# Optimization experiments

Measured on AMD Instinct MI355X. Metric: run time of the kernel, lower is better.

## Reference

```python
import jax, jax.numpy as jnp
import numpy as np

N_NODES = 50000
N_EDGES = 800000
DIM = 128
N_LAYERS = 5


def setup_inputs() -> dict:
    key = jax.random.key(0)
    k1, k2, k3, k4 = jax.random.split(key, 4)
    x = jax.random.normal(k1, (N_NODES, DIM), dtype=jnp.float32)
    edge_index = jax.random.randint(k2, (2, N_EDGES), 0, N_NODES, dtype=jnp.int64)
    # He-ish scale for stacked GCN layers so activations stay sane
    weights = jax.random.normal(k3, (N_LAYERS, DIM, DIM), dtype=jnp.float32) / jnp.sqrt(jnp.float32(DIM))
    biases = jax.random.normal(k4, (N_LAYERS, DIM), dtype=jnp.float32) * 0.01
    return {"x": x, "edge_index": edge_index, "weights": weights, "biases": biases}


def reference(x, edge_index, weights, biases):
    """5x (GCNConv -> ReLU). GCNConv: out = D^-1/2 (A+I) D^-1/2 (x W) + b."""
    n = x.shape[0]
    src, dst = edge_index[0], edge_index[1]
    # add self-loops (PyG GCNConv default)
    loop = jnp.arange(n, dtype=src.dtype)
    src_f = jnp.concatenate([src, loop])
    dst_f = jnp.concatenate([dst, loop])
    # symmetric normalization based on in-degree (incl. self loops)
    deg = jax.ops.segment_sum(jnp.ones(src_f.shape[0], dtype=x.dtype), dst_f, num_segments=n)
    dinv = jnp.where(deg > 0, jax.lax.rsqrt(deg), 0.0)
    norm = dinv[src_f] * dinv[dst_f]  # [E+N]

    for l in range(weights.shape[0]):
        h = x @ weights[l]                      # [N, D] dense transform
        msg = h[src_f] * norm[:, None]          # gather + scale  [E+N, D]
        x = jax.ops.segment_sum(msg, dst_f, num_segments=n) + biases[l]
        x = jax.nn.relu(x)
    return x
```

## Files before the change

kernel.cpp:

```cpp
#include <hip/hip_runtime.h>
#include <hip/hip_bf16.h>
#include <hip/hip_fp16.h>


#define GCN_DIM 128

typedef short bf16x8 __attribute__((ext_vector_type(8)));
typedef float f32x4 __attribute__((ext_vector_type(4)));

__device__ __forceinline__ unsigned short f2bf(float f) {
    unsigned int u = __float_as_uint(f);
    u += 0x7FFFu + ((u >> 16) & 1u);
    return (unsigned short)(u >> 16);
}
__device__ __forceinline__ float bf2f(unsigned short b) {
    return __uint_as_float(((unsigned int)b) << 16);
}
__device__ __forceinline__ float bflo(unsigned int p) { return __uint_as_float(p << 16); }
__device__ __forceinline__ float bfhi(unsigned int p) { return __uint_as_float(p & 0xFFFF0000u); }

__global__ void count_kernel(const int* __restrict__ dst, int* __restrict__ cnt,
                             int* __restrict__ rank, int E) {
    int e = blockIdx.x * 256 + threadIdx.x;
    if (e < E) rank[e] = atomicAdd(&cnt[dst[e]], 1);
}

__global__ __launch_bounds__(256) void scan_part_kernel(const int* __restrict__ cnt,
                                                        int* __restrict__ loc,
                                                        int* __restrict__ bsum, int n) {
    __shared__ int s[256];
    int t = threadIdx.x;
    int i0 = blockIdx.x * 1024 + t * 4;
    int v0 = (i0 + 0 < n) ? cnt[i0 + 0] : 0;
    int v1 = (i0 + 1 < n) ? cnt[i0 + 1] : 0;
    int v2 = (i0 + 2 < n) ? cnt[i0 + 2] : 0;
    int v3 = (i0 + 3 < n) ? cnt[i0 + 3] : 0;
    int tsum = v0 + v1 + v2 + v3;
    s[t] = tsum;
    __syncthreads();
    for (int d = 1; d < 256; d <<= 1) {
        int u = (t >= d) ? s[t - d] : 0;
        __syncthreads();
        s[t] += u;
        __syncthreads();
    }
    int base = s[t] - tsum;
    if (i0 + 0 < n) loc[i0 + 0] = base; base += v0;
    if (i0 + 1 < n) loc[i0 + 1] = base; base += v1;
    if (i0 + 2 < n) loc[i0 + 2] = base; base += v2;
    if (i0 + 3 < n) loc[i0 + 3] = base;
    if (t == 255) bsum[blockIdx.x] = s[255];
}

__global__ __launch_bounds__(256) void scan_top_kernel(int* __restrict__ bsum, int nb) {
    __shared__ int s[256];
    int t = threadIdx.x;
    int v = (t < nb) ? bsum[t] : 0;
    s[t] = v;
    __syncthreads();
    for (int d = 1; d < 256; d <<= 1) {
        int u = (t >= d) ? s[t - d] : 0;
        __syncthreads();
        s[t] += u;
        __syncthreads();
    }
    if (t < nb) bsum[t] = s[t] - v;
}

__global__ void scan_add_kernel(int* __restrict__ offs,
                                const int* __restrict__ bsum, const int* __restrict__ cnt,
                                float* __restrict__ dinv, int n, int E) {
    int i = blockIdx.x * 256 + threadIdx.x;
    if (i < n) {
        offs[i] = offs[i] + bsum[i >> 10];
        dinv[i] = rsqrtf((float)cnt[i] + 1.0f);
    }
    if (i == 0) offs[n] = E;
}

__global__ void fill_kernel(const int* __restrict__ src, const int* __restrict__ dst,
                            const float* __restrict__ dinv, const int* __restrict__ rank,
                            const int* __restrict__ offs,
                            unsigned int* __restrict__ edat, int E) {
    int e = blockIdx.x * 256 + threadIdx.x;
    if (e < E) {
        int d = dst[e];
        int s = src[e];
        int p = offs[d] + rank[e];
        unsigned short wb = __half_as_ushort(__float2half(dinv[s]));
        edat[p] = (unsigned int)s | ((unsigned int)wb << 16);
    }
}

__global__ void split_x_kernel(const float* __restrict__ x, unsigned short* __restrict__ xh,
                               unsigned short* __restrict__ xl, int total) {
    int i = (blockIdx.x * 256 + threadIdx.x) * 4;
    if (i >= total) return;
    float4 v = *(const float4*)&x[i];
    ushort4 h4, l4;
    h4.x = f2bf(v.x); l4.x = f2bf(v.x - bf2f(h4.x));
    h4.y = f2bf(v.y); l4.y = f2bf(v.y - bf2f(h4.y));
    h4.z = f2bf(v.z); l4.z = f2bf(v.z - bf2f(h4.z));
    h4.w = f2bf(v.w); l4.w = f2bf(v.w - bf2f(h4.w));
    *(ushort4*)&xh[i] = h4;
    *(ushort4*)&xl[i] = l4;
}

__global__ void wsplit_kernel(const float* __restrict__ Wall, unsigned short* __restrict__ Wfh,
                              unsigned short* __restrict__ Wfl, int total) {
    int idx = blockIdx.x * 256 + threadIdx.x;
    if (idx >= total) return;
    int l = idx >> 14;
    int rem = idx & 16383;
    int k = rem >> 7;
    int nn = rem & 127;
    float v = Wall[idx];
    unsigned short hi = f2bf(v);
    unsigned short lo = f2bf(v - bf2f(hi));
    int t = nn >> 4, ln = nn & 15;
    int ks = k >> 5, q = (k >> 3) & 3, j = k & 7;
    int o = ((((l << 5) | (t << 2) | ks) << 6) | (q << 4) | ln) * 8 + j;
    Wfh[o] = hi;
    Wfl[o] = lo;
}

__global__ __launch_bounds__(256) void gemm_mfma_kernel(
    const unsigned short* __restrict__ xh, const unsigned short* __restrict__ xl,
    const unsigned short* __restrict__ Wfh, const unsigned short* __restrict__ Wfl,
    unsigned short* __restrict__ h, int n) {
    __shared__ unsigned short ldsW[2][8192];
    int tid = threadIdx.x;
    int wave = tid >> 6, lane = tid & 63;
    int q = lane >> 4, ln = lane & 15;
    int rowbase = blockIdx.x * 64 + wave * 16;
    bf16x8 A[4][2];
    {
        int ar = rowbase + ln;
        if (ar >= n) ar = n - 1;
        size_t base = (size_t)ar * GCN_DIM;
#pragma unroll
        for (int ks = 0; ks < 4; ks++) {
            A[ks][0] = *(const bf16x8*)&xh[base + ks * 32 + q * 8];
            A[ks][1] = *(const bf16x8*)&xl[base + ks * 32 + q * 8];
        }
    }
    int node = rowbase + ln;
#pragma unroll
    for (int half = 0; half < 2; half++) {
        if (half) __syncthreads();
        {
            const uint4* gh = (const uint4*)(Wfh + half * 8192);
            const uint4* gl = (const uint4*)(Wfl + half * 8192);
            uint4* sh = (uint4*)ldsW[0];
            uint4* sl = (uint4*)ldsW[1];
#pragma unroll
            for (int r = 0; r < 4; r++) {
                sh[tid + 256 * r] = gh[tid + 256 * r];
                sl[tid + 256 * r] = gl[tid + 256 * r];
            }
        }
        __syncthreads();
#pragma unroll
        for (int tp = 0; tp < 2; tp++) {
            int tta = tp * 2, ttb = tp * 2 + 1;
            f32x4 accA = (f32x4)(0.f), accB = (f32x4)(0.f);
#pragma unroll
            for (int ks = 0; ks < 4; ks++) {
                int foA = ((tta * 4 + ks) * 64 + lane) * 8;
                int foB = ((ttb * 4 + ks) * 64 + lane) * 8;
                bf16x8 bhA = *(const bf16x8*)&ldsW[0][foA];
                bf16x8 blA = *(const bf16x8*)&ldsW[1][foA];
                bf16x8 bhB = *(const bf16x8*)&ldsW[0][foB];
                bf16x8 blB = *(const bf16x8*)&ldsW[1][foB];
                accA = __builtin_amdgcn_mfma_f32_16x16x32_bf16(bhA, A[ks][0], accA, 0, 0, 0);
                accB = __builtin_amdgcn_mfma_f32_16x16x32_bf16(bhB, A[ks][0], accB, 0, 0, 0);
                accA = __builtin_amdgcn_mfma_f32_16x16x32_bf16(bhA, A[ks][1], accA, 0, 0, 0);
                accB = __builtin_amdgcn_mfma_f32_16x16x32_bf16(bhB, A[ks][1], accB, 0, 0, 0);
                accA = __builtin_amdgcn_mfma_f32_16x16x32_bf16(blA, A[ks][0], accA, 0, 0, 0);
                accB = __builtin_amdgcn_mfma_f32_16x16x32_bf16(blB, A[ks][0], accB, 0, 0, 0);
            }
            if (node < n) {
                int ta = half * 4 + tta, tb = half * 4 + ttb;
                ushort4 oA, oB;
                oA.x = f2bf(accA[0]); oA.y = f2bf(accA[1]);
                oA.z = f2bf(accA[2]); oA.w = f2bf(accA[3]);
                oB.x = f2bf(accB[0]); oB.y = f2bf(accB[1]);
                oB.z = f2bf(accB[2]); oB.w = f2bf(accB[3]);
                *(ushort4*)&h[((size_t)ta * n + node) * 16 + q * 4] = oA;
                *(ushort4*)&h[((size_t)tb * n + node) * 16 + q * 4] = oB;
            }
        }
    }
}

__global__ __launch_bounds__(256) void agg_kernel(
    const unsigned short* __restrict__ h,
    const unsigned int* __restrict__ edat,
    const int* __restrict__ offs,
    const float* __restrict__ dinv, const float* __restrict__ bias,
    unsigned short* __restrict__ xh_out,
    unsigned short* __restrict__ xl_out,
    float* __restrict__ fout, int n) {
    int tid = threadIdx.x;
    int wave = tid >> 6, lane = tid & 63;
    int sub = lane >> 3, ln = lane & 7;
    int slice = blockIdx.x & 7;
    int node = (blockIdx.x >> 3) * 32 + wave * 8 + sub;
    if (node >= n) return;
    size_t sbase = (size_t)slice * n;
    int fo = ln * 2;
    float di = dinv[node];
    unsigned int sp = *(const unsigned int*)&h[(sbase + node) * 16 + fo];
    float ax0 = di * bflo(sp), ay0 = di * bfhi(sp);
    float ax1 = 0.f, ay1 = 0.f, ax2 = 0.f, ay2 = 0.f, ax3 = 0.f, ay3 = 0.f;
    int s = offs[node], e = offs[node + 1];
    int j = s;
    for (; j + 8 <= e; j += 8) {
        unsigned int v0 = edat[j], v1 = edat[j + 1], v2 = edat[j + 2], v3 = edat[j + 3];
        unsigned int v4 = edat[j + 4], v5 = edat[j + 5], v6 = edat[j + 6], v7 = edat[j + 7];
        unsigned int p0 = *(const unsigned int*)&h[(sbase + (v0 & 0xFFFFu)) * 16 + fo];
        unsigned int p1 = *(const unsigned int*)&h[(sbase + (v1 & 0xFFFFu)) * 16 + fo];
        unsigned int p2 = *(const unsigned int*)&h[(sbase + (v2 & 0xFFFFu)) * 16 + fo];
        unsigned int p3 = *(const unsigned int*)&h[(sbase + (v3 & 0xFFFFu)) * 16 + fo];
        unsigned int p4 = *(const unsigned int*)&h[(sbase + (v4 & 0xFFFFu)) * 16 + fo];
        unsigned int p5 = *(const unsigned int*)&h[(sbase + (v5 & 0xFFFFu)) * 16 + fo];
        unsigned int p6 = *(const unsigned int*)&h[(sbase + (v6 & 0xFFFFu)) * 16 + fo];
        unsigned int p7 = *(const unsigned int*)&h[(sbase + (v7 & 0xFFFFu)) * 16 + fo];
        float w0 = __half2float(__ushort_as_half((unsigned short)(v0 >> 16)));
        float w1 = __half2float(__ushort_as_half((unsigned short)(v1 >> 16)));
        float w2 = __half2float(__ushort_as_half((unsigned short)(v2 >> 16)));
        float w3 = __half2float(__ushort_as_half((unsigned short)(v3 >> 16)));
        float w4 = __half2float(__ushort_as_half((unsigned short)(v4 >> 16)));
        float w5 = __half2float(__ushort_as_half((unsigned short)(v5 >> 16)));
        float w6 = __half2float(__ushort_as_half((unsigned short)(v6 >> 16)));
        float w7 = __half2float(__ushort_as_half((unsigned short)(v7 >> 16)));
        ax0 = fmaf(w0, bflo(p0), ax0); ay0 = fmaf(w0, bfhi(p0), ay0);
        ax1 = fmaf(w1, bflo(p1), ax1); ay1 = fmaf(w1, bfhi(p1), ay1);
        ax2 = fmaf(w2, bflo(p2), ax2); ay2 = fmaf(w2, bfhi(p2), ay2);
        ax3 = fmaf(w3, bflo(p3), ax3); ay3 = fmaf(w3, bfhi(p3), ay3);
        ax0 = fmaf(w4, bflo(p4), ax0); ay0 = fmaf(w4, bfhi(p4), ay0);
        ax1 = fmaf(w5, bflo(p5), ax1); ay1 = fmaf(w5, bfhi(p5), ay1);
        ax2 = fmaf(w6, bflo(p6), ax2); ay2 = fmaf(w6, bfhi(p6), ay2);
        ax3 = fmaf(w7, bflo(p7), ax3); ay3 = fmaf(w7, bfhi(p7), ay3);
    }
    for (; j + 4 <= e; j += 4) {
        unsigned int v0 = edat[j], v1 = edat[j + 1], v2 = edat[j + 2], v3 = edat[j + 3];
        unsigned int p0 = *(const unsigned int*)&h[(sbase + (v0 & 0xFFFFu)) * 16 + fo];
        unsigned int p1 = *(const unsigned int*)&h[(sbase + (v1 & 0xFFFFu)) * 16 + fo];
        unsigned int p2 = *(const unsigned int*)&h[(sbase + (v2 & 0xFFFFu)) * 16 + fo];
        unsigned int p3 = *(const unsigned int*)&h[(sbase + (v3 & 0xFFFFu)) * 16 + fo];
        float w0 = __half2float(__ushort_as_half((unsigned short)(v0 >> 16)));
        float w1 = __half2float(__ushort_as_half((unsigned short)(v1 >> 16)));
        float w2 = __half2float(__ushort_as_half((unsigned short)(v2 >> 16)));
        float w3 = __half2float(__ushort_as_half((unsigned short)(v3 >> 16)));
        ax0 = fmaf(w0, bflo(p0), ax0); ay0 = fmaf(w0, bfhi(p0), ay0);
        ax1 = fmaf(w1, bflo(p1), ax1); ay1 = fmaf(w1, bfhi(p1), ay1);
        ax2 = fmaf(w2, bflo(p2), ax2); ay2 = fmaf(w2, bfhi(p2), ay2);
        ax3 = fmaf(w3, bflo(p3), ax3); ay3 = fmaf(w3, bfhi(p3), ay3);
    }
    for (; j < e; j++) {
        unsigned int v0 = edat[j];
        unsigned int p0 = *(const unsigned int*)&h[(sbase + (v0 & 0xFFFFu)) * 16 + fo];
        float w0 = __half2float(__ushort_as_half((unsigned short)(v0 >> 16)));
        ax0 = fmaf(w0, bflo(p0), ax0);
        ay0 = fmaf(w0, bfhi(p0), ay0);
    }
    float ax = (ax0 + ax1) + (ax2 + ax3);
    float ay = (ay0 + ay1) + (ay2 + ay3);
    int cg = slice * 16 + fo;
    float2 b = *(const float2*)&bias[cg];
    float rx = fmaxf(fmaf(di, ax, b.x), 0.f);
    float ry = fmaxf(fmaf(di, ay, b.y), 0.f);
    if (fout) {
        unsigned long long pv = (unsigned long long)__float_as_uint(rx) |
                                ((unsigned long long)__float_as_uint(ry) << 32);
        __builtin_nontemporal_store(pv, (unsigned long long*)&fout[(size_t)node * GCN_DIM + cg]);
    } else {
        unsigned short hx = f2bf(rx), hy = f2bf(ry);
        unsigned int hp = (unsigned int)hx | ((unsigned int)hy << 16);
        unsigned short lx = f2bf(rx - bf2f(hx)), ly = f2bf(ry - bf2f(hy));
        unsigned int lp = (unsigned int)lx | ((unsigned int)ly << 16);
        __builtin_nontemporal_store(hp, (unsigned int*)&xh_out[(size_t)node * GCN_DIM + cg]);
        __builtin_nontemporal_store(lp, (unsigned int*)&xl_out[(size_t)node * GCN_DIM + cg]);
    }
}

extern "C" void kernel_launch(void* const* d_in, const int* in_sizes, int n_in,
                              void* d_out, int out_size, void* d_ws, size_t ws_size,
                              hipStream_t stream) {
    const float* x0    = (const float*)d_in[0];
    const int*   edges = (const int*)d_in[1];
    const float* Wall  = (const float*)d_in[2];
    const float* Ball  = (const float*)d_in[3];
    float* out = (float*)d_out;

    const int n = in_sizes[0] / GCN_DIM;
    const int E = in_sizes[1] / 2;
    const int L = in_sizes[2] / (GCN_DIM * GCN_DIM);

    int*   cnt    = (int*)d_ws;
    float* dinv   = (float*)(cnt + n);
    int*   offs   = (int*)(dinv + n);
    int*   bsum   = offs + n + 16;
    int*   rank   = bsum + 64;
    unsigned int* edat = (unsigned int*)(rank + E);
    unsigned short* h   = (unsigned short*)(edat + E);
    unsigned short* xh  = h  + (size_t)n * GCN_DIM;
    unsigned short* xl  = xh + (size_t)n * GCN_DIM;
    unsigned short* Wfh = xl + (size_t)n * GCN_DIM;
    unsigned short* Wfl = Wfh + (size_t)L * GCN_DIM * GCN_DIM;

    const int* src = edges;
    const int* dst = edges + E;

    int nb_n = (n + 255) / 256;
    int nb_e = (E + 255) / 256;
    int nb_scan = (n + 1023) / 1024;

    hipMemsetAsync(cnt, 0, (size_t)n * sizeof(int), stream);
    count_kernel<<<nb_e, 256, 0, stream>>>(dst, cnt, rank, E);
    scan_part_kernel<<<nb_scan, 256, 0, stream>>>(cnt, offs, bsum, n);
    scan_top_kernel<<<1, 256, 0, stream>>>(bsum, nb_scan);
    scan_add_kernel<<<nb_n, 256, 0, stream>>>(offs, bsum, cnt, dinv, n, E);
    fill_kernel<<<nb_e, 256, 0, stream>>>(src, dst, dinv, rank, offs, edat, E);

    int xtotal = n * GCN_DIM;
    split_x_kernel<<<(xtotal / 4 + 255) / 256, 256, 0, stream>>>(x0, xh, xl, xtotal);
    int wtotal = L * GCN_DIM * GCN_DIM;
    wsplit_kernel<<<(wtotal + 255) / 256, 256, 0, stream>>>(Wall, Wfh, Wfl, wtotal);

    int gemm_blocks = (n + 63) / 64;
    int agg_blocks  = ((n + 31) / 32) * 8;

    for (int l = 0; l < L; l++) {
        gemm_mfma_kernel<<<gemm_blocks, 256, 0, stream>>>(
            xh, xl, Wfh + (size_t)l * GCN_DIM * GCN_DIM, Wfl + (size_t)l * GCN_DIM * GCN_DIM, h, n);
        agg_kernel<<<agg_blocks, 256, 0, stream>>>(
            h, edat, offs, dinv, Ball + (size_t)l * GCN_DIM,
            xh, xl, (l == L - 1) ? out : nullptr, n);
    }
}
```

Measured before the change: 414.2 us.

## Sort nodes by degree for aggregation and interleave hi/lo activation splits

Adds a counting sort of nodes by in-degree (capped at 127), so each aggregation wave handles nodes of similar degree and lanes within a wave diverge less. The bf16 hi/lo activation halves are interleaved into one buffer with 32-element chunks per slice, so the aggregation write and the GEMM A-load touch nearby memory. This costs three extra setup kernels and an indirection through the order array, and output stores become scattered by node id.

```diff
diff --git a/kernel.cpp b/kernel.cpp
--- a/kernel.cpp
+++ b/kernel.cpp
@@ -92,8 +92,52 @@
     }
 }
 
-__global__ void split_x_kernel(const float* __restrict__ x, unsigned short* __restrict__ xh,
-                               unsigned short* __restrict__ xl, int total) {
+__global__ __launch_bounds__(256) void dhist_kernel(const int* __restrict__ cnt,
+                                                    int* __restrict__ dhist,
+                                                    int* __restrict__ drank, int n) {
+    __shared__ int lhist[128];
+    __shared__ int lbase[128];
+    int t = threadIdx.x;
+    if (t < 128) lhist[t] = 0;
+    __syncthreads();
+    int i = blockIdx.x * 256 + t;
+    int d = 0, lr = 0;
+    if (i < n) {
+        d = min(cnt[i], 127);
+        lr = atomicAdd(&lhist[d], 1);
+    }
+    __syncthreads();
+    if (t < 128) lbase[t] = (lhist[t] > 0) ? atomicAdd(&dhist[t], lhist[t]) : 0;
+    __syncthreads();
+    if (i < n) drank[i] = lbase[d] + lr;
+}
+
+__global__ __launch_bounds__(128) void dscan_kernel(int* __restrict__ dhist) {
+    __shared__ int s[128];
+    int t = threadIdx.x;
+    int v = dhist[t];
+    s[t] = v;
+    __syncthreads();
+    for (int d = 1; d < 128; d <<= 1) {
+        int u = (t >= d) ? s[t - d] : 0;
+        __syncthreads();
+        s[t] += u;
+        __syncthreads();
+    }
+    dhist[t] = s[t] - v;
+}
+
+__global__ void dorder_kernel(const int* __restrict__ cnt, const int* __restrict__ dhist,
+                              const int* __restrict__ drank, int* __restrict__ order, int n) {
+    int i = blockIdx.x * 256 + threadIdx.x;
+    if (i < n) {
+        int d = min(cnt[i], 127);
+        order[dhist[d] + drank[i]] = i;
+    }
+}
+
+__global__ void split_x_kernel(const float* __restrict__ x, unsigned short* __restrict__ xs,
+                               int total) {
     int i = (blockIdx.x * 256 + threadIdx.x) * 4;
     if (i >= total) return;
     float4 v = *(const float4*)&x[i];
@@ -102,8 +146,11 @@
     h4.y = f2bf(v.y); l4.y = f2bf(v.y - bf2f(h4.y));
     h4.z = f2bf(v.z); l4.z = f2bf(v.z - bf2f(h4.z));
     h4.w = f2bf(v.w); l4.w = f2bf(v.w - bf2f(h4.w));
-    *(ushort4*)&xh[i] = h4;
-    *(ushort4*)&xl[i] = l4;
+    int node = i >> 7, k = i & 127;
+    int s = k >> 4, within = k & 15;
+    size_t base = (size_t)node * 256 + s * 32 + within;
+    *(ushort4*)&xs[base] = h4;
+    *(ushort4*)&xs[base + 16] = l4;
 }
 
 __global__ void wsplit_kernel(const float* __restrict__ Wall, unsigned short* __restrict__ Wfh,
@@ -125,7 +172,7 @@
 }
 
 __global__ __launch_bounds__(256) void gemm_mfma_kernel(
-    const unsigned short* __restrict__ xh, const unsigned short* __restrict__ xl,
+    const unsigned short* __restrict__ xs,
     const unsigned short* __restrict__ Wfh, const unsigned short* __restrict__ Wfl,
     unsigned short* __restrict__ h, int n) {
     __shared__ unsigned short ldsW[2][8192];
@@ -137,11 +184,13 @@
     {
         int ar = rowbase + ln;
         if (ar >= n) ar = n - 1;
-        size_t base = (size_t)ar * GCN_DIM;
+        size_t base = (size_t)ar * 256;
 #pragma unroll
         for (int ks = 0; ks < 4; ks++) {
-            A[ks][0] = *(const bf16x8*)&xh[base + ks * 32 + q * 8];
-            A[ks][1] = *(const bf16x8*)&xl[base + ks * 32 + q * 8];
+            int s = 2 * ks + (q >> 1);
+            int within = (q & 1) * 8;
+            A[ks][0] = *(const bf16x8*)&xs[base + s * 32 + within];
+            A[ks][1] = *(const bf16x8*)&xs[base + s * 32 + 16 + within];
         }
     }
     int node = rowbase + ln;
@@ -198,15 +247,16 @@
     const unsigned int* __restrict__ edat,
     const int* __restrict__ offs,
     const float* __restrict__ dinv, const float* __restrict__ bias,
-    unsigned short* __restrict__ xh_out,
-    unsigned short* __restrict__ xl_out,
+    const int* __restrict__ order,
+    unsigned short* __restrict__ xs_out,
     float* __restrict__ fout, int n) {
     int tid = threadIdx.x;
     int wave = tid >> 6, lane = tid & 63;
     int sub = lane >> 3, ln = lane & 7;
     int slice = blockIdx.x & 7;
-    int node = (blockIdx.x >> 3) * 32 + wave * 8 + sub;
-    if (node >= n) return;
+    int g = (blockIdx.x >> 3) * 32 + wave * 8 + sub;
+    if (g >= n) return;
+    int node = order[g];
     size_t sbase = (size_t)slice * n;
     int fo = ln * 2;
     float di = dinv[node];
@@ -280,8 +330,9 @@
         unsigned int hp = (unsigned int)hx | ((unsigned int)hy << 16);
         unsigned short lx = f2bf(rx - bf2f(hx)), ly = f2bf(ry - bf2f(hy));
         unsigned int lp = (unsigned int)lx | ((unsigned int)ly << 16);
-        __builtin_nontemporal_store(hp, (unsigned int*)&xh_out[(size_t)node * GCN_DIM + cg]);
-        __builtin_nontemporal_store(lp, (unsigned int*)&xl_out[(size_t)node * GCN_DIM + cg]);
+        size_t ob = (size_t)node * 256 + slice * 32 + fo;
+        __builtin_nontemporal_store(hp, (unsigned int*)&xs_out[ob]);
+        __builtin_nontemporal_store(lp, (unsigned int*)&xs_out[ob + 16]);
     }
 }
 
@@ -299,15 +350,17 @@
     const int L = in_sizes[2] / (GCN_DIM * GCN_DIM);
 
     int*   cnt    = (int*)d_ws;
-    float* dinv   = (float*)(cnt + n);
+    int*   dhist  = cnt + n;
+    float* dinv   = (float*)(dhist + 128);
     int*   offs   = (int*)(dinv + n);
     int*   bsum   = offs + n + 16;
-    int*   rank   = bsum + 64;
+    int*   drank  = bsum + 64;
+    int*   order  = drank + n;
+    int*   rank   = order + n;
     unsigned int* edat = (unsigned int*)(rank + E);
     unsigned short* h   = (unsigned short*)(edat + E);
-    unsigned short* xh  = h  + (size_t)n * GCN_DIM;
-    unsigned short* xl  = xh + (size_t)n * GCN_DIM;
-    unsigned short* Wfh = xl + (size_t)n * GCN_DIM;
+    unsigned short* xs  = h  + (size_t)n * GCN_DIM;
+    unsigned short* Wfh = xs + (size_t)n * 256;
     unsigned short* Wfl = Wfh + (size_t)L * GCN_DIM * GCN_DIM;
 
     const int* src = edges;
@@ -317,15 +370,18 @@
     int nb_e = (E + 255) / 256;
     int nb_scan = (n + 1023) / 1024;
 
-    hipMemsetAsync(cnt, 0, (size_t)n * sizeof(int), stream);
+    hipMemsetAsync(cnt, 0, ((size_t)n + 128) * sizeof(int), stream);
     count_kernel<<<nb_e, 256, 0, stream>>>(dst, cnt, rank, E);
     scan_part_kernel<<<nb_scan, 256, 0, stream>>>(cnt, offs, bsum, n);
     scan_top_kernel<<<1, 256, 0, stream>>>(bsum, nb_scan);
     scan_add_kernel<<<nb_n, 256, 0, stream>>>(offs, bsum, cnt, dinv, n, E);
     fill_kernel<<<nb_e, 256, 0, stream>>>(src, dst, dinv, rank, offs, edat, E);
+    dhist_kernel<<<nb_n, 256, 0, stream>>>(cnt, dhist, drank, n);
+    dscan_kernel<<<1, 128, 0, stream>>>(dhist);
+    dorder_kernel<<<nb_n, 256, 0, stream>>>(cnt, dhist, drank, order, n);
 
     int xtotal = n * GCN_DIM;
-    split_x_kernel<<<(xtotal / 4 + 255) / 256, 256, 0, stream>>>(x0, xh, xl, xtotal);
+    split_x_kernel<<<(xtotal / 4 + 255) / 256, 256, 0, stream>>>(x0, xs, xtotal);
     int wtotal = L * GCN_DIM * GCN_DIM;
     wsplit_kernel<<<(wtotal + 255) / 256, 256, 0, stream>>>(Wall, Wfh, Wfl, wtotal);
 
@@ -334,9 +390,9 @@
 
     for (int l = 0; l < L; l++) {
         gemm_mfma_kernel<<<gemm_blocks, 256, 0, stream>>>(
-            xh, xl, Wfh + (size_t)l * GCN_DIM * GCN_DIM, Wfl + (size_t)l * GCN_DIM * GCN_DIM, h, n);
+            xs, Wfh + (size_t)l * GCN_DIM * GCN_DIM, Wfl + (size_t)l * GCN_DIM * GCN_DIM, h, n);
         agg_kernel<<<agg_blocks, 256, 0, stream>>>(
-            h, edat, offs, dinv, Ball + (size_t)l * GCN_DIM,
-            xh, xl, (l == L - 1) ? out : nullptr, n);
-    }
-}
+            h, edat, offs, dinv, Ball + (size_t)l * GCN_DIM, order,
+            xs, (l == L - 1) ? out : nullptr, n);
+    }
+}
```

Result: slower. 443.5 us (+7.1%).
